# Optimization experiments

Measured on AMD Instinct MI355X. Metric: run time of the kernel, lower is better.

Reference implementation:

```python
import jax, jax.numpy as jnp
import numpy as np

HID, OUT, D = 256, 64, 128
N_ITEM, N_USER, E = 100000, 50000, 800000


def sage_conv(x_src, x_dst, src, dst, w_l, b_l, w_r, n_dst):
    # PyG SAGEConv (mean aggr): out = lin_l(mean_j x_src[j]) + lin_r(x_dst)
    msg = x_src[src]                                        # [E, d_src] gather
    agg = jax.ops.segment_sum(msg, dst, num_segments=n_dst)  # [n_dst, d_src]
    cnt = jax.ops.segment_sum(jnp.ones((src.shape[0],), x_src.dtype), dst,
                              num_segments=n_dst)
    mean = agg / jnp.clip(cnt, 1.0, None)[:, None]
    return mean @ w_l + b_l + x_dst @ w_r


def setup_inputs() -> dict:
    key = jax.random.key(0)
    ks = jax.random.split(key, 16)
    sc = lambda d: 1.0 / np.sqrt(d)
    inp = {
        "x_item": jax.random.normal(ks[0], (N_ITEM, D), jnp.float32),
        "x_user": jax.random.normal(ks[1], (N_USER, D), jnp.float32),
        "ei_ii_src": jax.random.randint(ks[2], (E,), 0, N_ITEM),
        "ei_ii_dst": jax.random.randint(ks[3], (E,), 0, N_ITEM),
        "ei_iu_src": jax.random.randint(ks[4], (E,), 0, N_ITEM),
        "ei_iu_dst": jax.random.randint(ks[5], (E,), 0, N_USER),
        # conv1: item->item, in (D, D) -> HID
        "w_l1": jax.random.normal(ks[6], (D, HID), jnp.float32) * sc(D),
        "b1": jnp.zeros((HID,), jnp.float32),
        "w_r1": jax.random.normal(ks[7], (D, HID), jnp.float32) * sc(D),
        # conv2: (item D, user D) -> HID
        "w_l2": jax.random.normal(ks[8], (D, HID), jnp.float32) * sc(D),
        "b2": jnp.zeros((HID,), jnp.float32),
        "w_r2": jax.random.normal(ks[9], (D, HID), jnp.float32) * sc(D),
        # conv3: (item HID, user HID) -> HID
        "w_l3": jax.random.normal(ks[10], (HID, HID), jnp.float32) * sc(HID),
        "b3": jnp.zeros((HID,), jnp.float32),
        "w_r3": jax.random.normal(ks[11], (HID, HID), jnp.float32) * sc(HID),
        # final linear HID -> OUT
        "w_lin": jax.random.normal(ks[12], (HID, OUT), jnp.float32) * sc(HID),
        "b_lin": jnp.zeros((OUT,), jnp.float32),
    }
    return inp


def reference(x_item, x_user, ei_ii_src, ei_ii_dst, ei_iu_src, ei_iu_dst,
              w_l1, b1, w_r1, w_l2, b2, w_r2, w_l3, b3, w_r3, w_lin, b_lin):
    item_x = jax.nn.relu(sage_conv(x_item, x_item, ei_ii_src, ei_ii_dst,
                                   w_l1, b1, w_r1, N_ITEM))
    user_x = jax.nn.relu(sage_conv(x_item, x_user, ei_iu_src, ei_iu_dst,
                                   w_l2, b2, w_r2, N_USER))
    user_x = jax.nn.relu(sage_conv(item_x, user_x, ei_iu_src, ei_iu_dst,
                                   w_l3, b3, w_r3, N_USER))
    return user_x @ w_lin + b_lin
```

## Files before the change

kernel.cpp:

```cpp
#include <hip/hip_runtime.h>
#include <hip/hip_bf16.h>

#define N_ITEM 100000
#define N_USER 50000
#define D_IN   128
#define HID    256
#define OUT_D  64
#define CAP    64

#define SCB   1024
#define CVIB  2048
#define CVUB  1024
#define PKB   136
#define PREP_GRID (SCB + CVIB + CVUB + PKB)

typedef __attribute__((ext_vector_type(8))) short bf16x8;
typedef __attribute__((ext_vector_type(4))) float f32x4;

__device__ inline float b2f(unsigned int h) {
    union { unsigned int u; float f; } c; c.u = h << 16; return c.f;
}
__device__ inline unsigned short f2b(float f) {
    unsigned int u = __builtin_bit_cast(unsigned int, f);
    u += 0x7fff + ((u >> 16) & 1);
    return (unsigned short)(u >> 16);
}

__device__ inline void pack_unit(const float* __restrict__ wl,
                                 const float* __restrict__ wr,
                                 int K, int NCv, unsigned short* __restrict__ dst,
                                 int u)
{
    int kb = u / NCv, col = u - kb * NCv;
    int colp = col ^ (kb & 7);
    unsigned short tmp[8];
    #pragma unroll
    for (int j = 0; j < 8; ++j) {
        int k = kb * 8 + j;
        float w = (k < K) ? wl[(size_t)k * NCv + col]
                          : wr[(size_t)(k - K) * NCv + col];
        tmp[j] = f2b(w);
    }
    *(uint4*)&dst[((size_t)kb * NCv + colp) * 8] = *(const uint4*)tmp;
}

__global__ __launch_bounds__(256) void prep_kernel(
    const int* __restrict__ ii_src, const int* __restrict__ ii_dst,
    const int* __restrict__ iu_src, const int* __restrict__ iu_dst,
    int* __restrict__ cur_i, int* __restrict__ cur_u,
    int* __restrict__ slot_ii, int* __restrict__ slot_iu, int E,
    const float* __restrict__ x_item, const float* __restrict__ x_user,
    unsigned short* __restrict__ Acat1, unsigned short* __restrict__ Acat2,
    const float* __restrict__ wl1, const float* __restrict__ wr1,
    const float* __restrict__ wl2, const float* __restrict__ wr2,
    const float* __restrict__ wl3, const float* __restrict__ wr3,
    const float* __restrict__ wlin,
    unsigned short* __restrict__ Wp1, unsigned short* __restrict__ Wp2,
    unsigned short* __restrict__ Wp3, unsigned short* __restrict__ Wpl)
{
    int b = blockIdx.x;
    if (b < SCB) {
        const int NT = SCB * 256;
        int e = b * 256 + threadIdx.x;
        for (; e + 3 * NT < E; e += 4 * NT) {
            int d[8], s[8], p[8];
            #pragma unroll
            for (int u = 0; u < 4; ++u) {
                d[u]     = ii_dst[e + u * NT]; s[u]     = ii_src[e + u * NT];
                d[u + 4] = iu_dst[e + u * NT]; s[u + 4] = iu_src[e + u * NT];
            }
            #pragma unroll
            for (int u = 0; u < 4; ++u) p[u] = atomicAdd(&cur_i[d[u]], 1);
            #pragma unroll
            for (int u = 4; u < 8; ++u) p[u] = atomicAdd(&cur_u[d[u]], 1);
            #pragma unroll
            for (int u = 0; u < 4; ++u)
                if (p[u] < CAP) slot_ii[d[u] * CAP + p[u]] = s[u];
            #pragma unroll
            for (int u = 4; u < 8; ++u)
                if (p[u] < CAP) slot_iu[d[u] * CAP + p[u]] = s[u];
        }
        for (; e < E; e += NT) {
            int d0 = ii_dst[e], s0 = ii_src[e];
            int p0 = atomicAdd(&cur_i[d0], 1);
            if (p0 < CAP) slot_ii[d0 * CAP + p0] = s0;
            int d1 = iu_dst[e], s1 = iu_src[e];
            int p1 = atomicAdd(&cur_u[d1], 1);
            if (p1 < CAP) slot_iu[d1 * CAP + p1] = s1;
        }
    } else if (b < SCB + CVIB) {
        const int STR = CVIB * 256;
        for (int u = (b - SCB) * 256 + threadIdx.x; u < N_ITEM * 32; u += STR) {
            int row = u >> 5, c4 = (u & 31) * 4;
            float4 v = *(const float4*)&x_item[(size_t)row * 128 + c4];
            ushort4 o;
            o.x = f2b(v.x); o.y = f2b(v.y); o.z = f2b(v.z); o.w = f2b(v.w);
            *(ushort4*)&Acat1[(size_t)row * 256 + 128 + c4] = o;
        }
    } else if (b < SCB + CVIB + CVUB) {
        const int STR = CVUB * 256;
        for (int u = (b - SCB - CVIB) * 256 + threadIdx.x; u < N_USER * 32; u += STR) {
            int row = u >> 5, c4 = (u & 31) * 4;
            float4 v = *(const float4*)&x_user[(size_t)row * 128 + c4];
            ushort4 o;
            o.x = f2b(v.x); o.y = f2b(v.y); o.z = f2b(v.z); o.w = f2b(v.w);
            *(ushort4*)&Acat2[(size_t)row * 256 + 128 + c4] = o;
        }
    } else {
        int t = (b - SCB - CVIB - CVUB) * 256 + threadIdx.x;
        if (t < 8192)       pack_unit(wl1, wr1, 128, 256, Wp1, t);
        else if (t < 16384) pack_unit(wl2, wr2, 128, 256, Wp2, t - 8192);
        else if (t < 32768) pack_unit(wl3, wr3, 256, 256, Wp3, t - 16384);
        else if (t < 34816) pack_unit(wlin, wlin, 256, 64, Wpl, t - 32768);
    }
}

__global__ __launch_bounds__(256) void agg12_kernel(
    const unsigned short* __restrict__ xsrc,
    const int* __restrict__ slot_ii, const int* __restrict__ cur_i,
    const int* __restrict__ slot_iu, const int* __restrict__ cur_u,
    unsigned short* __restrict__ Acat1, unsigned short* __restrict__ Acat2)
{
    int b = blockIdx.x;
    const int* sl; int num; unsigned short* dst;
    if (b < 25000) {
        int row = b * 4 + (threadIdx.x >> 6);
        sl  = slot_ii + (size_t)row * CAP;
        num = min(cur_i[row], CAP);
        dst = Acat1 + (size_t)row * 256;
    } else {
        int row = (b - 25000) * 4 + (threadIdx.x >> 6);
        sl  = slot_iu + (size_t)row * CAP;
        num = min(cur_u[row], CAP);
        dst = Acat2 + (size_t)row * 256;
    }
    int lane = threadIdx.x & 63;
    const unsigned short* xb = xsrc + (size_t)lane * 2;
    float acc0 = 0.f, acc1 = 0.f;

    int j = 0;
    for (; j + 8 <= num; j += 8) {
        int s[8];
        #pragma unroll
        for (int u = 0; u < 8; ++u) s[u] = sl[j + u];
        unsigned int v[8];
        #pragma unroll
        for (int u = 0; u < 8; ++u)
            v[u] = *(const unsigned int*)(xb + (size_t)s[u] * 256);
        #pragma unroll
        for (int u = 0; u < 8; ++u) {
            acc0 += b2f(v[u] & 0xffffu);
            acc1 += b2f(v[u] >> 16);
        }
    }
    for (; j < num; ++j) {
        unsigned int v = *(const unsigned int*)(xb + (size_t)sl[j] * 256);
        acc0 += b2f(v & 0xffffu);
        acc1 += b2f(v >> 16);
    }

    float sc = 1.0f / fmaxf((float)num, 1.0f);
    unsigned int w = (unsigned int)f2b(acc0 * sc) |
                     ((unsigned int)f2b(acc1 * sc) << 16);
    *(unsigned int*)(dst + lane * 2) = w;
}

__global__ __launch_bounds__(256) void agg_mean256(
    const unsigned short* __restrict__ x, int ldx,
    const int* __restrict__ slots, const int* __restrict__ cnt,
    unsigned short* __restrict__ dst, int ldd, int nrows)
{
    int row = blockIdx.x * 4 + (threadIdx.x >> 6);
    if (row >= nrows) return;
    int lane = threadIdx.x & 63;
    const int* sl = slots + (size_t)row * CAP;
    int num = min(cnt[row], CAP);
    const unsigned short* xb = x + (size_t)lane * 4;
    float acc[4] = {};

    int j = 0;
    for (; j + 8 <= num; j += 8) {
        int s[8];
        #pragma unroll
        for (int u = 0; u < 8; ++u) s[u] = sl[j + u];
        uint2 v[8];
        #pragma unroll
        for (int u = 0; u < 8; ++u)
            v[u] = *(const uint2*)(xb + (size_t)s[u] * ldx);
        #pragma unroll
        for (int u = 0; u < 8; ++u) {
            acc[0] += b2f(v[u].x & 0xffffu);
            acc[1] += b2f(v[u].x >> 16);
            acc[2] += b2f(v[u].y & 0xffffu);
            acc[3] += b2f(v[u].y >> 16);
        }
    }
    for (; j < num; ++j) {
        uint2 v = *(const uint2*)(xb + (size_t)sl[j] * ldx);
        acc[0] += b2f(v.x & 0xffffu);
        acc[1] += b2f(v.x >> 16);
        acc[2] += b2f(v.y & 0xffffu);
        acc[3] += b2f(v.y >> 16);
    }

    float sc = 1.0f / fmaxf((float)num, 1.0f);
    uint2 w;
    w.x = (unsigned int)f2b(acc[0] * sc) | ((unsigned int)f2b(acc[1] * sc) << 16);
    w.y = (unsigned int)f2b(acc[2] * sc) | ((unsigned int)f2b(acc[3] * sc) << 16);
    *(uint2*)(dst + (size_t)row * ldd + lane * 4) = w;
}

template <int NC, int WM, int WN, bool OUT_BF16, bool RELU>
__global__ __launch_bounds__(512) void gemm_mfma(
    const unsigned short* __restrict__ A, int lda,
    const unsigned short* __restrict__ Wp,
    const float* __restrict__ bias,
    void* __restrict__ Cout, int ldc, int col_off,
    int nrows, int nkt)
{
    constexpr int BM = 128;
    constexpr int MR = WM / 16, NR = WN / 16;
    constexpr int NWC = NC / WN;
    __shared__ unsigned short As[BM * 64];
    __shared__ unsigned short Bs[64 * NC];

    const int tid  = threadIdx.x;
    const int wave = tid >> 6;
    const int lane = tid & 63;
    const int row0 = blockIdx.x * BM;
    const int wr = wave / NWC;
    const int wc = wave % NWC;

    f32x4 acc[MR][NR];
    #pragma unroll
    for (int m = 0; m < MR; ++m)
        #pragma unroll
        for (int n = 0; n < NR; ++n)
            acc[m][n] = (f32x4){0.f, 0.f, 0.f, 0.f};

    for (int kt = 0; kt < nkt; ++kt) {
        #pragma unroll
        for (int c = 0; c < 2; ++c) {
            int i = wave * 2 + c;
            int rl = 8 * i + (lane >> 3);
            int kc = (lane & 7) ^ (lane >> 3);
            const unsigned short* g =
                A + (size_t)(row0 + rl) * lda + kt * 64 + kc * 8;
            __builtin_amdgcn_global_load_lds(
                (const __attribute__((address_space(1))) void*)g,
                (__attribute__((address_space(3))) void*)(As + i * 512), 16, 0, 0);
        }
        constexpr int BCALLS = (64 * NC * 2) / 1024;
        constexpr int PW = BCALLS / 8;
        #pragma unroll
        for (int c = 0; c < PW; ++c) {
            int j = wave * PW + c;
            const unsigned short* g =
                Wp + (size_t)kt * (8 * NC * 8) + (size_t)j * 512 + lane * 8;
            __builtin_amdgcn_global_load_lds(
                (const __attribute__((address_space(1))) void*)g,
                (__attribute__((address_space(3))) void*)(Bs + j * 512), 16, 0, 0);
        }
        __syncthreads();

        #pragma unroll
        for (int kk = 0; kk < 2; ++kk) {
            bf16x8 af[MR], bfr[NR];
            #pragma unroll
            for (int m = 0; m < MR; ++m) {
                int row = wr * WM + m * 16 + (lane & 15);
                int kc = ((kk * 4) + (lane >> 4)) ^ (lane & 7);
                af[m] = *(const bf16x8*)(As + row * 64 + kc * 8);
            }
            #pragma unroll
            for (int n = 0; n < NR; ++n) {
                int kb = kk * 4 + (lane >> 4);
                int col = (wc * WN + n * 16 + (lane & 15)) ^ (kb & 7);
                bfr[n] = *(const bf16x8*)(Bs + (kb * NC + col) * 8);
            }
            #pragma unroll
            for (int m = 0; m < MR; ++m)
                #pragma unroll
                for (int n = 0; n < NR; ++n)
                    acc[m][n] = __builtin_amdgcn_mfma_f32_16x16x32_bf16(
                        af[m], bfr[n], acc[m][n], 0, 0, 0);
        }
        __syncthreads();
    }

    #pragma unroll
    for (int n = 0; n < NR; ++n) {
        int col = wc * WN + n * 16 + (lane & 15);
        float bv = bias[col];
        #pragma unroll
        for (int m = 0; m < MR; ++m) {
            #pragma unroll
            for (int j = 0; j < 4; ++j) {
                int row = row0 + wr * WM + m * 16 + (lane >> 4) * 4 + j;
                if (row < nrows) {
                    float v = acc[m][n][j] + bv;
                    if (RELU) v = fmaxf(v, 0.f);
                    if (OUT_BF16)
                        ((unsigned short*)Cout)[(size_t)row * ldc + col_off + col] = f2b(v);
                    else
                        ((float*)Cout)[(size_t)row * ldc + col_off + col] = v;
                }
            }
        }
    }
}

extern "C" void kernel_launch(void* const* d_in, const int* in_sizes, int n_in,
                              void* d_out, int out_size, void* d_ws, size_t ws_size,
                              hipStream_t stream)
{
    const float* x_item = (const float*)d_in[0];
    const float* x_user = (const float*)d_in[1];
    const int* ii_src   = (const int*)d_in[2];
    const int* ii_dst   = (const int*)d_in[3];
    const int* iu_src   = (const int*)d_in[4];
    const int* iu_dst   = (const int*)d_in[5];
    const float* w_l1 = (const float*)d_in[6];
    const float* b1   = (const float*)d_in[7];
    const float* w_r1 = (const float*)d_in[8];
    const float* w_l2 = (const float*)d_in[9];
    const float* b2   = (const float*)d_in[10];
    const float* w_r2 = (const float*)d_in[11];
    const float* w_l3 = (const float*)d_in[12];
    const float* b3   = (const float*)d_in[13];
    const float* w_r3 = (const float*)d_in[14];
    const float* w_lin = (const float*)d_in[15];
    const float* b_lin = (const float*)d_in[16];
    float* out = (float*)d_out;

    const int E = in_sizes[2];
    const int NIP = 100096;
    const int NUP = 50048;

    int* cur_i   = (int*)d_ws;
    int* cur_u   = cur_i + 100352;
    int* slot_ii = cur_u + 50176;
    int* slot_iu = slot_ii + N_ITEM * CAP;

    unsigned short* Acat1  = (unsigned short*)(slot_iu + N_USER * CAP);
    unsigned short* item_x = Acat1  + (size_t)NIP * 256;
    unsigned short* Acat2  = item_x + (size_t)NIP * 256;
    unsigned short* Acat3  = Acat2  + (size_t)NUP * 256;
    unsigned short* ux3    = Acat3  + (size_t)NUP * 512;
    unsigned short* Wp1    = ux3    + (size_t)NUP * 256;
    unsigned short* Wp2    = Wp1 + 65536;
    unsigned short* Wp3    = Wp2 + 65536;
    unsigned short* Wpl    = Wp3 + 131072;

    hipMemsetAsync(cur_i, 0, (size_t)150528 * 4, stream);

    prep_kernel<<<PREP_GRID, 256, 0, stream>>>(
        ii_src, ii_dst, iu_src, iu_dst, cur_i, cur_u, slot_ii, slot_iu, E,
        x_item, x_user, Acat1, Acat2,
        w_l1, w_r1, w_l2, w_r2, w_l3, w_r3, w_lin,
        Wp1, Wp2, Wp3, Wpl);

    agg12_kernel<<<37500, 256, 0, stream>>>(
        Acat1 + 128, slot_ii, cur_i, slot_iu, cur_u, Acat1, Acat2);

    gemm_mfma<256, 64, 64, true, true><<<NIP / 128, 512, 0, stream>>>(
        Acat1, 256, Wp1, b1, item_x, 256, 0, N_ITEM, 4);

    gemm_mfma<256, 64, 64, true, true><<<NUP / 128, 512, 0, stream>>>(
        Acat2, 256, Wp2, b2, Acat3, 512, 256, N_USER, 4);

    agg_mean256<<<(N_USER + 3) / 4, 256, 0, stream>>>(
        item_x, 256, slot_iu, cur_u, Acat3, 512, N_USER);

    gemm_mfma<256, 64, 64, true, true><<<NUP / 128, 512, 0, stream>>>(
        Acat3, 512, Wp3, b3, ux3, 256, 0, N_USER, 8);

    gemm_mfma<64, 16, 64, false, false><<<NUP / 128, 512, 0, stream>>>(
        ux3, 256, Wpl, b_lin, out, 64, 0, N_USER, 4);
}
```

Before: 368.3 us.

## Pad edge counters, widen gather lanes, and fuse conv2 GEMM with layer-3 aggregation

Each per-destination counter now sits 16 ints apart to reduce atomic contention and false sharing while the edges are bucketed, and slot writes use nontemporal stores. The scatter grid shrinks from 1024 to 256 blocks. The gather kernels now use a half-wave (32 lanes) per row with wider vector loads (8 or 16 bytes), so each block covers more rows. The conv2 GEMM and the layer-3 mean aggregation are merged into one launch whose blocks split by index, so the two independent jobs can overlap and one launch is saved. The cost is a larger counter memset and mixed block roles with different resource needs in one kernel.

```diff
diff --git a/kernel.cpp b/kernel.cpp
--- a/kernel.cpp
+++ b/kernel.cpp
@@ -7,12 +7,16 @@
 #define HID    256
 #define OUT_D  64
 #define CAP    64
-
-#define SCB   1024
+#define CPAD   16
+
+#define SCB   256
 #define CVIB  2048
 #define CVUB  1024
 #define PKB   136
 #define PREP_GRID (SCB + CVIB + CVUB + PKB)
+
+#define C2B   391
+#define A3B   3125
 
 typedef __attribute__((ext_vector_type(8))) short bf16x8;
 typedef __attribute__((ext_vector_type(4))) float f32x4;
@@ -70,23 +74,25 @@
                 d[u + 4] = iu_dst[e + u * NT]; s[u + 4] = iu_src[e + u * NT];
             }
             #pragma unroll
-            for (int u = 0; u < 4; ++u) p[u] = atomicAdd(&cur_i[d[u]], 1);
-            #pragma unroll
-            for (int u = 4; u < 8; ++u) p[u] = atomicAdd(&cur_u[d[u]], 1);
+            for (int u = 0; u < 4; ++u) p[u] = atomicAdd(&cur_i[d[u] * CPAD], 1);
+            #pragma unroll
+            for (int u = 4; u < 8; ++u) p[u] = atomicAdd(&cur_u[d[u] * CPAD], 1);
             #pragma unroll
             for (int u = 0; u < 4; ++u)
-                if (p[u] < CAP) slot_ii[d[u] * CAP + p[u]] = s[u];
+                if (p[u] < CAP)
+                    __builtin_nontemporal_store(s[u], &slot_ii[d[u] * CAP + p[u]]);
             #pragma unroll
             for (int u = 4; u < 8; ++u)
-                if (p[u] < CAP) slot_iu[d[u] * CAP + p[u]] = s[u];
+                if (p[u] < CAP)
+                    __builtin_nontemporal_store(s[u], &slot_iu[d[u] * CAP + p[u]]);
         }
         for (; e < E; e += NT) {
             int d0 = ii_dst[e], s0 = ii_src[e];
-            int p0 = atomicAdd(&cur_i[d0], 1);
-            if (p0 < CAP) slot_ii[d0 * CAP + p0] = s0;
+            int p0 = atomicAdd(&cur_i[d0 * CPAD], 1);
+            if (p0 < CAP) __builtin_nontemporal_store(s0, &slot_ii[d0 * CAP + p0]);
             int d1 = iu_dst[e], s1 = iu_src[e];
-            int p1 = atomicAdd(&cur_u[d1], 1);
-            if (p1 < CAP) slot_iu[d1 * CAP + p1] = s1;
+            int p1 = atomicAdd(&cur_u[d1 * CPAD], 1);
+            if (p1 < CAP) __builtin_nontemporal_store(s1, &slot_iu[d1 * CAP + p1]);
         }
     } else if (b < SCB + CVIB) {
         const int STR = CVIB * 256;
@@ -122,71 +128,32 @@
     unsigned short* __restrict__ Acat1, unsigned short* __restrict__ Acat2)
 {
     int b = blockIdx.x;
+    int sub = threadIdx.x >> 5;
     const int* sl; int num; unsigned short* dst;
-    if (b < 25000) {
-        int row = b * 4 + (threadIdx.x >> 6);
+    if (b < 12500) {
+        int row = b * 8 + sub;
         sl  = slot_ii + (size_t)row * CAP;
-        num = min(cur_i[row], CAP);
+        num = min(cur_i[(size_t)row * CPAD], CAP);
         dst = Acat1 + (size_t)row * 256;
     } else {
-        int row = (b - 25000) * 4 + (threadIdx.x >> 6);
+        int row = (b - 12500) * 8 + sub;
         sl  = slot_iu + (size_t)row * CAP;
-        num = min(cur_u[row], CAP);
+        num = min(cur_u[(size_t)row * CPAD], CAP);
         dst = Acat2 + (size_t)row * 256;
     }
-    int lane = threadIdx.x & 63;
-    const unsigned short* xb = xsrc + (size_t)lane * 2;
-    float acc0 = 0.f, acc1 = 0.f;
+    int hl = threadIdx.x & 31;
+    const unsigned short* xb = xsrc + hl * 4;
+    float acc[4] = {};
 
     int j = 0;
     for (; j + 8 <= num; j += 8) {
         int s[8];
         #pragma unroll
         for (int u = 0; u < 8; ++u) s[u] = sl[j + u];
-        unsigned int v[8];
+        uint2 v[8];
         #pragma unroll
         for (int u = 0; u < 8; ++u)
-            v[u] = *(const unsigned int*)(xb + (size_t)s[u] * 256);
-        #pragma unroll
-        for (int u = 0; u < 8; ++u) {
-            acc0 += b2f(v[u] & 0xffffu);
-            acc1 += b2f(v[u] >> 16);
-        }
-    }
-    for (; j < num; ++j) {
-        unsigned int v = *(const unsigned int*)(xb + (size_t)sl[j] * 256);
-        acc0 += b2f(v & 0xffffu);
-        acc1 += b2f(v >> 16);
-    }
-
-    float sc = 1.0f / fmaxf((float)num, 1.0f);
-    unsigned int w = (unsigned int)f2b(acc0 * sc) |
-                     ((unsigned int)f2b(acc1 * sc) << 16);
-    *(unsigned int*)(dst + lane * 2) = w;
-}
-
-__global__ __launch_bounds__(256) void agg_mean256(
-    const unsigned short* __restrict__ x, int ldx,
-    const int* __restrict__ slots, const int* __restrict__ cnt,
-    unsigned short* __restrict__ dst, int ldd, int nrows)
-{
-    int row = blockIdx.x * 4 + (threadIdx.x >> 6);
-    if (row >= nrows) return;
-    int lane = threadIdx.x & 63;
-    const int* sl = slots + (size_t)row * CAP;
-    int num = min(cnt[row], CAP);
-    const unsigned short* xb = x + (size_t)lane * 4;
-    float acc[4] = {};
-
-    int j = 0;
-    for (; j + 8 <= num; j += 8) {
-        int s[8];
-        #pragma unroll
-        for (int u = 0; u < 8; ++u) s[u] = sl[j + u];
-        uint2 v[8];
-        #pragma unroll
-        for (int u = 0; u < 8; ++u)
-            v[u] = *(const uint2*)(xb + (size_t)s[u] * ldx);
+            v[u] = *(const uint2*)(xb + (size_t)s[u] * 256);
         #pragma unroll
         for (int u = 0; u < 8; ++u) {
             acc[0] += b2f(v[u].x & 0xffffu);
@@ -196,7 +163,7 @@
         }
     }
     for (; j < num; ++j) {
-        uint2 v = *(const uint2*)(xb + (size_t)sl[j] * ldx);
+        uint2 v = *(const uint2*)(xb + (size_t)sl[j] * 256);
         acc[0] += b2f(v.x & 0xffffu);
         acc[1] += b2f(v.x >> 16);
         acc[2] += b2f(v.y & 0xffffu);
@@ -207,11 +174,12 @@
     uint2 w;
     w.x = (unsigned int)f2b(acc[0] * sc) | ((unsigned int)f2b(acc[1] * sc) << 16);
     w.y = (unsigned int)f2b(acc[2] * sc) | ((unsigned int)f2b(acc[3] * sc) << 16);
-    *(uint2*)(dst + (size_t)row * ldd + lane * 4) = w;
+    *(uint2*)(dst + hl * 4) = w;
 }
 
 template <int NC, int WM, int WN, bool OUT_BF16, bool RELU>
-__global__ __launch_bounds__(512) void gemm_mfma(
+__device__ __forceinline__ void gemm_body(
+    int bid,
     const unsigned short* __restrict__ A, int lda,
     const unsigned short* __restrict__ Wp,
     const float* __restrict__ bias,
@@ -227,7 +195,7 @@
     const int tid  = threadIdx.x;
     const int wave = tid >> 6;
     const int lane = tid & 63;
-    const int row0 = blockIdx.x * BM;
+    const int row0 = bid * BM;
     const int wr = wave / NWC;
     const int wc = wave % NWC;
 
@@ -308,6 +276,81 @@
             }
         }
     }
+}
+
+template <int NC, int WM, int WN, bool OUT_BF16, bool RELU>
+__global__ __launch_bounds__(512) void gemm_mfma(
+    const unsigned short* __restrict__ A, int lda,
+    const unsigned short* __restrict__ Wp,
+    const float* __restrict__ bias,
+    void* __restrict__ Cout, int ldc, int col_off,
+    int nrows, int nkt)
+{
+    gemm_body<NC, WM, WN, OUT_BF16, RELU>(blockIdx.x, A, lda, Wp, bias,
+                                          Cout, ldc, col_off, nrows, nkt);
+}
+
+__global__ __launch_bounds__(512) void conv2_agg3_kernel(
+    const unsigned short* __restrict__ Acat2,
+    const unsigned short* __restrict__ Wp2,
+    const float* __restrict__ b2,
+    unsigned short* __restrict__ Acat3,
+    const unsigned short* __restrict__ item_x,
+    const int* __restrict__ slot_iu, const int* __restrict__ cur_u)
+{
+    if (blockIdx.x < C2B) {
+        gemm_body<256, 64, 64, true, true>(blockIdx.x, Acat2, 256, Wp2, b2,
+                                           Acat3, 512, 256, N_USER, 4);
+        return;
+    }
+    int b = blockIdx.x - C2B;
+    int row = b * 16 + (threadIdx.x >> 5);
+    int hl = threadIdx.x & 31;
+    const int* sl = slot_iu + (size_t)row * CAP;
+    int num = min(cur_u[(size_t)row * CPAD], CAP);
+    const unsigned short* xb = item_x + hl * 8;
+    float acc[8] = {};
+
+    int j = 0;
+    for (; j + 8 <= num; j += 8) {
+        int s[8];
+        #pragma unroll
+        for (int u = 0; u < 8; ++u) s[u] = sl[j + u];
+        uint4 v[8];
+        #pragma unroll
+        for (int u = 0; u < 8; ++u)
+            v[u] = *(const uint4*)(xb + (size_t)s[u] * 256);
+        #pragma unroll
+        for (int u = 0; u < 8; ++u) {
+            acc[0] += b2f(v[u].x & 0xffffu);
+            acc[1] += b2f(v[u].x >> 16);
+            acc[2] += b2f(v[u].y & 0xffffu);
+            acc[3] += b2f(v[u].y >> 16);
+            acc[4] += b2f(v[u].z & 0xffffu);
+            acc[5] += b2f(v[u].z >> 16);
+            acc[6] += b2f(v[u].w & 0xffffu);
+            acc[7] += b2f(v[u].w >> 16);
+        }
+    }
+    for (; j < num; ++j) {
+        uint4 v = *(const uint4*)(xb + (size_t)sl[j] * 256);
+        acc[0] += b2f(v.x & 0xffffu);
+        acc[1] += b2f(v.x >> 16);
+        acc[2] += b2f(v.y & 0xffffu);
+        acc[3] += b2f(v.y >> 16);
+        acc[4] += b2f(v.z & 0xffffu);
+        acc[5] += b2f(v.z >> 16);
+        acc[6] += b2f(v.w & 0xffffu);
+        acc[7] += b2f(v.w >> 16);
+    }
+
+    float sc = 1.0f / fmaxf((float)num, 1.0f);
+    uint4 w;
+    w.x = (unsigned int)f2b(acc[0] * sc) | ((unsigned int)f2b(acc[1] * sc) << 16);
+    w.y = (unsigned int)f2b(acc[2] * sc) | ((unsigned int)f2b(acc[3] * sc) << 16);
+    w.z = (unsigned int)f2b(acc[4] * sc) | ((unsigned int)f2b(acc[5] * sc) << 16);
+    w.w = (unsigned int)f2b(acc[6] * sc) | ((unsigned int)f2b(acc[7] * sc) << 16);
+    *(uint4*)(Acat3 + (size_t)row * 512 + hl * 8) = w;
 }
 
 extern "C" void kernel_launch(void* const* d_in, const int* in_sizes, int n_in,
@@ -338,11 +381,11 @@
     const int NUP = 50048;
 
     int* cur_i   = (int*)d_ws;
-    int* cur_u   = cur_i + 100352;
-    int* slot_ii = cur_u + 50176;
-    int* slot_iu = slot_ii + N_ITEM * CAP;
-
-    unsigned short* Acat1  = (unsigned short*)(slot_iu + N_USER * CAP);
+    int* cur_u   = cur_i + (size_t)N_ITEM * CPAD;
+    int* slot_ii = cur_u + (size_t)N_USER * CPAD;
+    int* slot_iu = slot_ii + (size_t)N_ITEM * CAP;
+
+    unsigned short* Acat1  = (unsigned short*)(slot_iu + (size_t)N_USER * CAP);
     unsigned short* item_x = Acat1  + (size_t)NIP * 256;
     unsigned short* Acat2  = item_x + (size_t)NIP * 256;
     unsigned short* Acat3  = Acat2  + (size_t)NUP * 256;
@@ -352,7 +395,7 @@
     unsigned short* Wp3    = Wp2 + 65536;
     unsigned short* Wpl    = Wp3 + 131072;
 
-    hipMemsetAsync(cur_i, 0, (size_t)150528 * 4, stream);
+    hipMemsetAsync(cur_i, 0, (size_t)(N_ITEM + N_USER) * CPAD * 4, stream);
 
     prep_kernel<<<PREP_GRID, 256, 0, stream>>>(
         ii_src, ii_dst, iu_src, iu_dst, cur_i, cur_u, slot_ii, slot_iu, E,
@@ -360,17 +403,14 @@
         w_l1, w_r1, w_l2, w_r2, w_l3, w_r3, w_lin,
         Wp1, Wp2, Wp3, Wpl);
 
-    agg12_kernel<<<37500, 256, 0, stream>>>(
+    agg12_kernel<<<18750, 256, 0, stream>>>(
         Acat1 + 128, slot_ii, cur_i, slot_iu, cur_u, Acat1, Acat2);
 
     gemm_mfma<256, 64, 64, true, true><<<NIP / 128, 512, 0, stream>>>(
         Acat1, 256, Wp1, b1, item_x, 256, 0, N_ITEM, 4);
 
-    gemm_mfma<256, 64, 64, true, true><<<NUP / 128, 512, 0, stream>>>(
-        Acat2, 256, Wp2, b2, Acat3, 512, 256, N_USER, 4);
-
-    agg_mean256<<<(N_USER + 3) / 4, 256, 0, stream>>>(
-        item_x, 256, slot_iu, cur_u, Acat3, 512, N_USER);
+    conv2_agg3_kernel<<<C2B + A3B, 512, 0, stream>>>(
+        Acat2, Wp2, b2, Acat3, item_x, slot_iu, cur_u);
 
     gemm_mfma<256, 64, 64, true, true><<<NUP / 128, 512, 0, stream>>>(
         Acat3, 512, Wp3, b3, ux3, 256, 0, N_USER, 8);
```

New measurement: 386.3 us. +4.9%, slower.
